# Kernel optimization log

Measured on AMD Instinct MI355X. Metric: run time of the kernel, lower is better.

Reference implementation:

```python
import jax, jax.numpy as jnp
import numpy as np

N = 50000          # nodes
E = 800000         # edges
D_IN, D_HID, D_OUT = 256, 128, 64
NUM_GRAPHS = 16
BN_EPS = 1e-5


def gcn_conv(x, src, dst, W, b, n_nodes):
    """PyG GCNConv: add self-loops, sym-normalized aggregation, then bias."""
    loop = jnp.arange(n_nodes, dtype=src.dtype)
    s = jnp.concatenate([src, loop])
    d = jnp.concatenate([dst, loop])
    deg = jax.ops.segment_sum(jnp.ones_like(s, dtype=x.dtype), d, num_segments=n_nodes)
    dinv = jax.lax.rsqrt(jnp.maximum(deg, 1.0))  # deg >= 1 due to self-loops
    norm = dinv[s] * dinv[d]                      # [E+N]
    h = x @ W                                     # [N, out]
    msg = h[s] * norm[:, None]                    # gather + scale
    out = jax.ops.segment_sum(msg, d, num_segments=n_nodes)
    return out + b


def batch_norm(x, gamma, beta):
    mu = jnp.mean(x, axis=0)
    var = jnp.mean(jnp.square(x - mu), axis=0)
    return (x - mu) * jax.lax.rsqrt(var + BN_EPS) * gamma + beta


def setup_inputs() -> dict:
    key = jax.random.key(0)
    ks = jax.random.split(key, 10)
    x = jax.random.normal(ks[0], (N, D_IN), dtype=jnp.float32)
    edge_index = jax.random.randint(ks[1], (2, E), 0, N, dtype=jnp.int64)
    batch = jnp.sort(jax.random.randint(ks[2], (N,), 0, NUM_GRAPHS, dtype=jnp.int64))
    def glorot(k, fan_in, fan_out):
        lim = np.sqrt(6.0 / (fan_in + fan_out))
        return jax.random.uniform(k, (fan_in, fan_out), jnp.float32, -lim, lim)
    return {
        "x": x, "edge_index": edge_index, "batch": batch,
        "W1": glorot(ks[3], D_IN, D_HID),  "b1": jnp.zeros((D_HID,), jnp.float32),
        "W2": glorot(ks[4], D_HID, D_HID), "b2": jnp.zeros((D_HID,), jnp.float32),
        "W3": glorot(ks[5], D_HID, D_OUT), "b3": jnp.zeros((D_OUT,), jnp.float32),
        "g1": jnp.ones((D_HID,), jnp.float32), "be1": jnp.zeros((D_HID,), jnp.float32),
        "g2": jnp.ones((D_HID,), jnp.float32), "be2": jnp.zeros((D_HID,), jnp.float32),
    }


def reference(x, edge_index, batch, W1, b1, W2, b2, W3, b3, g1, be1, g2, be2):
    src, dst = edge_index[0], edge_index[1]
    n = x.shape[0]
    h = gcn_conv(x, src, dst, W1, b1, n)
    h = jax.nn.relu(batch_norm(h, g1, be1))
    h = gcn_conv(h, src, dst, W2, b2, n)
    h = jax.nn.relu(batch_norm(h, g2, be2))
    h = gcn_conv(h, src, dst, W3, b3, n)          # [N, D_OUT]
    # global mean pool over graph ids
    sums = jax.ops.segment_sum(h, batch, num_segments=NUM_GRAPHS)
    cnts = jax.ops.segment_sum(jnp.ones((n,), h.dtype), batch, num_segments=NUM_GRAPHS)
    return sums / jnp.maximum(cnts, 1.0)[:, None]  # [NUM_GRAPHS, D_OUT]
```

## Files before the change

kernel.cpp:

```cpp
#include <hip/hip_runtime.h>
#include <hip/hip_bf16.h>

#define D_IN   256
#define D_HID  128
#define D_OUT_ 64
#define NGRAPH 16
#define BN_EPS 1e-5f

#define SCAN_TPB 256
#define SCAN_VPT 4

typedef __attribute__((ext_vector_type(8))) short short8;
typedef __attribute__((ext_vector_type(4))) float floatx4;

__device__ __forceinline__ unsigned short f2bf(float x) {
    unsigned u = __float_as_uint(x);
    return (unsigned short)((u + 0x7fffu + ((u >> 16) & 1u)) >> 16);
}
__device__ __forceinline__ unsigned pack2bf(float lo, float hi) {
    return (unsigned)f2bf(lo) | ((unsigned)f2bf(hi) << 16);
}
__device__ __forceinline__ void bf2_decode(unsigned u, float& lo, float& hi) {
    lo = __uint_as_float(u << 16);
    hi = __uint_as_float(u & 0xffff0000u);
}
__device__ __forceinline__ void accum8(float* acc, uint4 qv, float wt) {
    float f0,f1,f2,f3,f4,f5,f6,f7;
    bf2_decode(qv.x, f0, f1); bf2_decode(qv.y, f2, f3);
    bf2_decode(qv.z, f4, f5); bf2_decode(qv.w, f6, f7);
    acc[0]=fmaf(f0,wt,acc[0]); acc[1]=fmaf(f1,wt,acc[1]);
    acc[2]=fmaf(f2,wt,acc[2]); acc[3]=fmaf(f3,wt,acc[3]);
    acc[4]=fmaf(f4,wt,acc[4]); acc[5]=fmaf(f5,wt,acc[5]);
    acc[6]=fmaf(f6,wt,acc[6]); acc[7]=fmaf(f7,wt,acc[7]);
}

__global__ void count_deg_kernel(const int* __restrict__ dst, int E, int* __restrict__ deg) {
    int e = blockIdx.x * blockDim.x + threadIdx.x;
    if (e < E) atomicAdd(&deg[dst[e]], 1);
}

__global__ void dinv_kernel(const int* __restrict__ deg, int N, float* __restrict__ dinv) {
    int v = blockIdx.x * blockDim.x + threadIdx.x;
    if (v < N) dinv[v] = rsqrtf((float)(deg[v] + 1));
}

__global__ void block_sum_kernel(const int* __restrict__ deg, int N, int* __restrict__ bsum) {
    __shared__ int red[SCAN_TPB];
    int t = threadIdx.x;
    int base = blockIdx.x * (SCAN_TPB * SCAN_VPT) + t;
    int s = 0;
    #pragma unroll
    for (int i = 0; i < SCAN_VPT; ++i) {
        int idx = base + i * SCAN_TPB;
        if (idx < N) s += deg[idx];
    }
    red[t] = s;
    __syncthreads();
    for (int off = SCAN_TPB / 2; off > 0; off >>= 1) {
        if (t < off) red[t] += red[t + off];
        __syncthreads();
    }
    if (t == 0) bsum[blockIdx.x] = red[0];
}

__global__ void scan_bsum_kernel(const int* __restrict__ bsum, int NB,
                                 int* __restrict__ bprefix,
                                 int* __restrict__ rowstart, int N, int E) {
    __shared__ int part[SCAN_TPB];
    int t = threadIdx.x;
    int s = (t < NB) ? bsum[t] : 0;
    part[t] = s;
    __syncthreads();
    for (int off = 1; off < SCAN_TPB; off <<= 1) {
        int x = (t >= off) ? part[t - off] : 0;
        __syncthreads();
        part[t] += x;
        __syncthreads();
    }
    if (t < NB) bprefix[t] = part[t] - s;
    if (t == 0) rowstart[N] = E;
}

__global__ void local_scan_kernel(const int* __restrict__ deg, int N,
                                  const int* __restrict__ bprefix,
                                  int* __restrict__ rowstart) {
    __shared__ int part[SCAN_TPB];
    int t = threadIdx.x;
    int base = blockIdx.x * (SCAN_TPB * SCAN_VPT) + t * SCAN_VPT;
    int v[SCAN_VPT];
    int s = 0;
    #pragma unroll
    for (int i = 0; i < SCAN_VPT; ++i) {
        v[i] = (base + i < N) ? deg[base + i] : 0;
        s += v[i];
    }
    part[t] = s;
    __syncthreads();
    for (int off = 1; off < SCAN_TPB; off <<= 1) {
        int x = (t >= off) ? part[t - off] : 0;
        __syncthreads();
        part[t] += x;
        __syncthreads();
    }
    int excl = part[t] - s + bprefix[blockIdx.x];
    #pragma unroll
    for (int i = 0; i < SCAN_VPT; ++i) {
        if (base + i < N) rowstart[base + i] = excl;
        excl += v[i];
    }
}

__global__ void wprep_kernel(const float* __restrict__ W, int K, int NOUT,
                             unsigned short* __restrict__ Wt) {
    int idx = blockIdx.x * blockDim.x + threadIdx.x;
    if (idx >= K * NOUT) return;
    int k = idx / NOUT, n = idx - k * NOUT;
    Wt[(size_t)n * K + k] = f2bf(W[idx]);
}

template<int K, int NOUT, int FUSE, int ABF16>
__device__ __forceinline__ void gemm_body(
        int bid, const void* __restrict__ Aptr, const unsigned short* __restrict__ Wt,
        unsigned short* __restrict__ Cb, int M,
        const float* __restrict__ scale, const float* __restrict__ shift) {
    constexpr int NT = NOUT / 16;
    constexpr int KS = K / 32;
    int lane = threadIdx.x & 63;
    int wave = threadIdx.x >> 6;
    int col  = lane & 15;
    int quad = lane >> 4;
    int kq   = quad * 8;
    int row  = bid * 64 + wave * 16 + col;
    int rowc = min(row, M - 1);

    short8 afr[KS];
    if (ABF16) {
        const unsigned short* Ab = (const unsigned short*)Aptr;
        uint4 q[KS];
        #pragma unroll
        for (int i = 0; i < KS; ++i)
            q[i] = *(const uint4*)&Ab[(size_t)rowc * K + i * 32 + kq];
        #pragma unroll
        for (int i = 0; i < KS; ++i) {
            if (FUSE) {
                int kb = i * 32 + kq;
                float f0,f1,f2,f3,f4,f5,f6,f7;
                bf2_decode(q[i].x, f0, f1); bf2_decode(q[i].y, f2, f3);
                bf2_decode(q[i].z, f4, f5); bf2_decode(q[i].w, f6, f7);
                float4 sc0 = *(const float4*)&scale[kb];
                float4 sc1 = *(const float4*)&scale[kb + 4];
                float4 sh0 = *(const float4*)&shift[kb];
                float4 sh1 = *(const float4*)&shift[kb + 4];
                f0 = fmaxf(0.f, fmaf(f0, sc0.x, sh0.x));
                f1 = fmaxf(0.f, fmaf(f1, sc0.y, sh0.y));
                f2 = fmaxf(0.f, fmaf(f2, sc0.z, sh0.z));
                f3 = fmaxf(0.f, fmaf(f3, sc0.w, sh0.w));
                f4 = fmaxf(0.f, fmaf(f4, sc1.x, sh1.x));
                f5 = fmaxf(0.f, fmaf(f5, sc1.y, sh1.y));
                f6 = fmaxf(0.f, fmaf(f6, sc1.z, sh1.z));
                f7 = fmaxf(0.f, fmaf(f7, sc1.w, sh1.w));
                uint4 p;
                p.x = pack2bf(f0, f1); p.y = pack2bf(f2, f3);
                p.z = pack2bf(f4, f5); p.w = pack2bf(f6, f7);
                afr[i] = __builtin_bit_cast(short8, p);
            } else {
                afr[i] = __builtin_bit_cast(short8, q[i]);
            }
        }
    } else {
        const float* Af = (const float*)Aptr;
        float4 a0[KS], a1[KS];
        #pragma unroll
        for (int i = 0; i < KS; ++i) {
            a0[i] = *(const float4*)&Af[(size_t)rowc * K + i * 32 + kq];
            a1[i] = *(const float4*)&Af[(size_t)rowc * K + i * 32 + kq + 4];
        }
        #pragma unroll
        for (int i = 0; i < KS; ++i) {
            uint4 p;
            p.x = pack2bf(a0[i].x, a0[i].y); p.y = pack2bf(a0[i].z, a0[i].w);
            p.z = pack2bf(a1[i].x, a1[i].y); p.w = pack2bf(a1[i].z, a1[i].w);
            afr[i] = __builtin_bit_cast(short8, p);
        }
    }

    floatx4 acc[NT];
    #pragma unroll
    for (int nt = 0; nt < NT; ++nt) acc[nt] = (floatx4){0.f, 0.f, 0.f, 0.f};

    #pragma unroll
    for (int i = 0; i < KS; ++i) {
        #pragma unroll
        for (int nt = 0; nt < NT; ++nt) {
            short8 bfrag = *(const short8*)&Wt[(size_t)(nt * 16 + col) * K + i * 32 + kq];
            acc[nt] = __builtin_amdgcn_mfma_f32_16x16x32_bf16(afr[i], bfrag, acc[nt], 0, 0, 0);
        }
    }

    int obase = bid * 64 + wave * 16 + quad * 4;
    #pragma unroll
    for (int r = 0; r < 4; ++r) {
        int orow = obase + r;
        if (orow < M) {
            #pragma unroll
            for (int nt = 0; nt < NT; ++nt)
                Cb[(size_t)orow * NOUT + nt * 16 + col] = f2bf(acc[nt][r]);
        }
    }
}

template<int K, int NOUT, int FUSE, int ABF16>
__global__ __launch_bounds__(256) void gemm_mfma_kernel(
        const void* __restrict__ Aptr, const unsigned short* __restrict__ Wt,
        unsigned short* __restrict__ Cb, int M,
        const float* __restrict__ scale, const float* __restrict__ shift) {
    gemm_body<K, NOUT, FUSE, ABF16>(blockIdx.x, Aptr, Wt, Cb, M, scale, shift);
}

__global__ __launch_bounds__(256) void gemm1_scatter_kernel(
        const float* __restrict__ x, const unsigned short* __restrict__ Wt1,
        unsigned short* __restrict__ Cb, int M, int GB,
        const int* __restrict__ src, const int* __restrict__ dst, int E,
        const int* __restrict__ rowstart, int* __restrict__ cursor,
        const float* __restrict__ dinv, int2* __restrict__ csr) {
    if ((int)blockIdx.x < GB) {
        gemm_body<D_IN, D_HID, 0, 0>(blockIdx.x, x, Wt1, Cb, M, nullptr, nullptr);
    } else {
        int e = ((int)blockIdx.x - GB) * 256 + threadIdx.x;
        if (e < E) {
            int s = src[e], d = dst[e];
            int pos = rowstart[d] + atomicAdd(&cursor[d], 1);
            csr[pos] = make_int2(s, __float_as_int(dinv[s] * dinv[d]));
        }
    }
}

template<int D>
__global__ __launch_bounds__(256) void agg_bf16_kernel(
        const unsigned short* __restrict__ h, const float* __restrict__ dinv,
        const int* __restrict__ rowstart, const int2* __restrict__ csr,
        const float* __restrict__ bias,
        unsigned short* __restrict__ outb, int N) {
    constexpr int LPR = D / 8;
    constexpr int RPB = 256 / LPR;
    int lane = threadIdx.x & (LPR - 1);
    int r    = threadIdx.x / LPR;
    int v = blockIdx.x * RPB + r;
    if (v >= N) return;
    int c0 = lane * 8;
    const unsigned short* hc = h + c0;

    float acc[8];
    {
        float dv = dinv[v];
        float w = dv * dv;
        uint4 q = *(const uint4*)&hc[(size_t)v * D];
        float4 b0 = *(const float4*)&bias[c0];
        float4 b1 = *(const float4*)&bias[c0 + 4];
        acc[0]=b0.x; acc[1]=b0.y; acc[2]=b0.z; acc[3]=b0.w;
        acc[4]=b1.x; acc[5]=b1.y; acc[6]=b1.z; acc[7]=b1.w;
        accum8(acc, q, w);
    }

    int j  = rowstart[v];
    int j1 = rowstart[v + 1];
    for (; j + 4 <= j1; j += 4) {
        int2 r0 = csr[j],     r1 = csr[j + 1];
        int2 r2 = csr[j + 2], r3 = csr[j + 3];
        uint4 q0 = *(const uint4*)&hc[(size_t)r0.x * D];
        uint4 q1 = *(const uint4*)&hc[(size_t)r1.x * D];
        uint4 q2 = *(const uint4*)&hc[(size_t)r2.x * D];
        uint4 q3 = *(const uint4*)&hc[(size_t)r3.x * D];
        accum8(acc, q0, __int_as_float(r0.y)); accum8(acc, q1, __int_as_float(r1.y));
        accum8(acc, q2, __int_as_float(r2.y)); accum8(acc, q3, __int_as_float(r3.y));
    }
    for (; j < j1; ++j) {
        int2 rc = csr[j];
        uint4 q = *(const uint4*)&hc[(size_t)rc.x * D];
        accum8(acc, q, __int_as_float(rc.y));
    }

    uint4 o;
    o.x = pack2bf(acc[0], acc[1]); o.y = pack2bf(acc[2], acc[3]);
    o.z = pack2bf(acc[4], acc[5]); o.w = pack2bf(acc[6], acc[7]);
    *(uint4*)&outb[(size_t)v * D + c0] = o;
}

__global__ void bn_stats_bf16_kernel(const unsigned short* __restrict__ x, int N,
                                     float* __restrict__ sums, float* __restrict__ sumsq) {
    __shared__ float ls0[256], ls1[256], lq0[256], lq1[256];
    int pr = threadIdx.x & 63;
    int rg = threadIdx.x >> 6;
    float s0=0.f, s1=0.f, q0=0.f, q1=0.f;
    for (int v = blockIdx.x * 4 + rg; v < N; v += gridDim.x * 4) {
        unsigned u = *(const unsigned*)&x[(size_t)v * 128 + pr * 2];
        float lo, hi; bf2_decode(u, lo, hi);
        s0 += lo; s1 += hi;
        q0 = fmaf(lo, lo, q0); q1 = fmaf(hi, hi, q1);
    }
    ls0[threadIdx.x]=s0; ls1[threadIdx.x]=s1; lq0[threadIdx.x]=q0; lq1[threadIdx.x]=q1;
    __syncthreads();
    if (threadIdx.x < 64) {
        int pp = threadIdx.x;
        float a0=0,a1=0,b0=0,b1=0;
        #pragma unroll
        for (int g = 0; g < 4; ++g) {
            a0 += ls0[g*64+pp]; a1 += ls1[g*64+pp];
            b0 += lq0[g*64+pp]; b1 += lq1[g*64+pp];
        }
        atomicAdd(&sums[pp*2],  a0); atomicAdd(&sums[pp*2+1],  a1);
        atomicAdd(&sumsq[pp*2], b0); atomicAdd(&sumsq[pp*2+1], b1);
    }
}

__global__ void bn_final_kernel(const float* __restrict__ sums, const float* __restrict__ sumsq,
                                const float* __restrict__ g, const float* __restrict__ be,
                                int N, float* __restrict__ scale, float* __restrict__ shift) {
    int c = threadIdx.x;
    float inv_n = 1.0f / (float)N;
    float mu  = sums[c] * inv_n;
    float var = sumsq[c] * inv_n - mu * mu;
    float sc  = g[c] * rsqrtf(var + BN_EPS);
    scale[c] = sc;
    shift[c] = fmaf(-mu, sc, be[c]);
}

__global__ void pool_bf16_kernel(const unsigned short* __restrict__ x,
                                 const int* __restrict__ batch, int N,
                                 float* __restrict__ psum, int* __restrict__ pcnt) {
    __shared__ float ls[NGRAPH * 64];
    __shared__ int   lc[NGRAPH];
    for (int i = threadIdx.x; i < NGRAPH * 64; i += blockDim.x) ls[i] = 0.f;
    if (threadIdx.x < NGRAPH) lc[threadIdx.x] = 0;
    __syncthreads();
    int total = N * 32;
    for (int idx = blockIdx.x * blockDim.x + threadIdx.x; idx < total;
         idx += gridDim.x * blockDim.x) {
        int v = idx >> 5, cp = idx & 31;
        unsigned u = *(const unsigned*)&x[(size_t)v * 64 + cp * 2];
        float lo, hi; bf2_decode(u, lo, hi);
        int g = batch[v];
        atomicAdd(&ls[g * 64 + cp * 2],     lo);
        atomicAdd(&ls[g * 64 + cp * 2 + 1], hi);
        if (cp == 0) atomicAdd(&lc[g], 1);
    }
    __syncthreads();
    for (int i = threadIdx.x; i < NGRAPH * 64; i += blockDim.x) atomicAdd(&psum[i], ls[i]);
    if (threadIdx.x < NGRAPH) atomicAdd(&pcnt[threadIdx.x], lc[threadIdx.x]);
}

__global__ void pool_final_kernel(const float* __restrict__ psum, const int* __restrict__ pcnt,
                                  float* __restrict__ out) {
    int i = threadIdx.x;
    int g = i >> 6;
    float cnt = (float)max(pcnt[g], 1);
    out[i] = psum[i] / cnt;
}

extern "C" void kernel_launch(void* const* d_in, const int* in_sizes, int n_in,
                              void* d_out, int out_size, void* d_ws, size_t ws_size,
                              hipStream_t stream) {
    const float* x   = (const float*)d_in[0];
    const int*   ei  = (const int*)d_in[1];
    const int*   bat = (const int*)d_in[2];
    const float* W1  = (const float*)d_in[3];
    const float* b1  = (const float*)d_in[4];
    const float* W2  = (const float*)d_in[5];
    const float* b2  = (const float*)d_in[6];
    const float* W3  = (const float*)d_in[7];
    const float* b3  = (const float*)d_in[8];
    const float* g1  = (const float*)d_in[9];
    const float* be1 = (const float*)d_in[10];
    const float* g2  = (const float*)d_in[11];
    const float* be2 = (const float*)d_in[12];
    float* out = (float*)d_out;

    int N = in_sizes[0] / D_IN;
    int E = in_sizes[1] / 2;
    const int* src = ei;
    const int* dst = ei + E;

    char* p = (char*)d_ws;
    auto alloc = [&](size_t bytes) { char* r = p; p += (bytes + 255) & ~(size_t)255; return r; };
    int NB = (N + SCAN_TPB * SCAN_VPT - 1) / (SCAN_TPB * SCAN_VPT);
    int*   deg      = (int*)  alloc((size_t)N * 4);
    int*   rowstart = (int*)  alloc((size_t)(N + 1) * 4);
    int*   cursor   = (int*)  alloc((size_t)N * 4);
    float* dinv     = (float*)alloc((size_t)N * 4);
    int*   bsum     = (int*)  alloc((size_t)NB * 4);
    int*   bprefix  = (int*)  alloc((size_t)NB * 4);
    int2*  csr      = (int2*) alloc((size_t)E * 8);
    unsigned short* hb16   = (unsigned short*)alloc((size_t)N * 128 * 2);
    unsigned short* aggb16 = (unsigned short*)alloc((size_t)N * 128 * 2);
    unsigned short* Wt1 = (unsigned short*)alloc((size_t)D_HID * D_IN * 2);
    unsigned short* Wt2 = (unsigned short*)alloc((size_t)D_HID * D_HID * 2);
    unsigned short* Wt3 = (unsigned short*)alloc((size_t)D_OUT_ * D_HID * 2);
    float* sums     = (float*)alloc(128 * 4);
    float* sumsq    = (float*)alloc(128 * 4);
    float* scl      = (float*)alloc(128 * 4);
    float* shf      = (float*)alloc(128 * 4);
    float* psum     = (float*)alloc(NGRAPH * 64 * 4);
    int*   pcnt     = (int*)  alloc(NGRAPH * 4);

    int tpb = 256;
    int ebl = (E + tpb - 1) / tpb;
    int nbl = (N + tpb - 1) / tpb;
    int gblocks = (N + 63) / 64;

    wprep_kernel<<<(D_IN * D_HID + 255) / 256, 256, 0, stream>>>(W1, D_IN, D_HID, Wt1);
    wprep_kernel<<<(D_HID * D_HID + 255) / 256, 256, 0, stream>>>(W2, D_HID, D_HID, Wt2);
    wprep_kernel<<<(D_HID * D_OUT_ + 255) / 256, 256, 0, stream>>>(W3, D_HID, D_OUT_, Wt3);

    (void)hipMemsetAsync(deg, 0, (size_t)N * 4, stream);
    (void)hipMemsetAsync(cursor, 0, (size_t)N * 4, stream);
    count_deg_kernel<<<ebl, tpb, 0, stream>>>(dst, E, deg);
    dinv_kernel<<<nbl, tpb, 0, stream>>>(deg, N, dinv);
    block_sum_kernel<<<NB, SCAN_TPB, 0, stream>>>(deg, N, bsum);
    scan_bsum_kernel<<<1, SCAN_TPB, 0, stream>>>(bsum, NB, bprefix, rowstart, N, E);
    local_scan_kernel<<<NB, SCAN_TPB, 0, stream>>>(deg, N, bprefix, rowstart);

    gemm1_scatter_kernel<<<gblocks + ebl, 256, 0, stream>>>(
        x, Wt1, hb16, N, gblocks, src, dst, E, rowstart, cursor, dinv, csr);

    agg_bf16_kernel<D_HID><<<(N + 15) / 16, 256, 0, stream>>>(
        hb16, dinv, rowstart, csr, b1, aggb16, N);
    (void)hipMemsetAsync(sums, 0, 128 * 4, stream);
    (void)hipMemsetAsync(sumsq, 0, 128 * 4, stream);
    bn_stats_bf16_kernel<<<256, 256, 0, stream>>>(aggb16, N, sums, sumsq);
    bn_final_kernel<<<1, 128, 0, stream>>>(sums, sumsq, g1, be1, N, scl, shf);

    gemm_mfma_kernel<D_HID, D_HID, 1, 1><<<gblocks, 256, 0, stream>>>(
        aggb16, Wt2, hb16, N, scl, shf);
    agg_bf16_kernel<D_HID><<<(N + 15) / 16, 256, 0, stream>>>(
        hb16, dinv, rowstart, csr, b2, aggb16, N);
    (void)hipMemsetAsync(sums, 0, 128 * 4, stream);
    (void)hipMemsetAsync(sumsq, 0, 128 * 4, stream);
    bn_stats_bf16_kernel<<<256, 256, 0, stream>>>(aggb16, N, sums, sumsq);
    bn_final_kernel<<<1, 128, 0, stream>>>(sums, sumsq, g2, be2, N, scl, shf);

    gemm_mfma_kernel<D_HID, D_OUT_, 1, 1><<<gblocks, 256, 0, stream>>>(
        aggb16, Wt3, hb16, N, scl, shf);
    agg_bf16_kernel<D_OUT_><<<(N + 31) / 32, 256, 0, stream>>>(
        hb16, dinv, rowstart, csr, b3, aggb16, N);

    (void)hipMemsetAsync(psum, 0, NGRAPH * 64 * 4, stream);
    (void)hipMemsetAsync(pcnt, 0, NGRAPH * 4, stream);
    pool_bf16_kernel<<<256, 256, 0, stream>>>(aggb16, bat, N, psum, pcnt);
    pool_final_kernel<<<1, NGRAPH * 64, 0, stream>>>(psum, pcnt, out);
}
```

Measured before the change: 419.3 us.

## Shrink CSR to source ids, fold BN finalize into GEMM, batch scatter

The CSR entries drop the precomputed edge weight and store only the source index. The aggregation kernels now rebuild each weight from dinv[src]*dinv[dst], which halves CSR traffic and removes the dinv gathers from the scatter. The separate bn_final kernel launches are removed: each fused GEMM block computes scale and shift from the sums into shared memory. The edge scatter now handles four edges per thread, and its blocks are placed before the GEMM blocks. The cost is an extra random dinv gather per edge in every aggregation pass and a redundant per-block BN finalize.

```diff
diff --git a/kernel.cpp b/kernel.cpp
--- a/kernel.cpp
+++ b/kernel.cpp
@@ -122,9 +122,23 @@
 __device__ __forceinline__ void gemm_body(
         int bid, const void* __restrict__ Aptr, const unsigned short* __restrict__ Wt,
         unsigned short* __restrict__ Cb, int M,
-        const float* __restrict__ scale, const float* __restrict__ shift) {
+        const float* __restrict__ sums, const float* __restrict__ sumsq,
+        const float* __restrict__ gam, const float* __restrict__ bet, float invN) {
     constexpr int NT = NOUT / 16;
     constexpr int KS = K / 32;
+    __shared__ float s_sc[FUSE ? K : 1];
+    __shared__ float s_sh[FUSE ? K : 1];
+    if (FUSE) {
+        int t = threadIdx.x;
+        if (t < K) {
+            float mu  = sums[t] * invN;
+            float var = sumsq[t] * invN - mu * mu;
+            float sc  = gam[t] * rsqrtf(var + BN_EPS);
+            s_sc[t] = sc;
+            s_sh[t] = fmaf(-mu, sc, bet[t]);
+        }
+        __syncthreads();
+    }
     int lane = threadIdx.x & 63;
     int wave = threadIdx.x >> 6;
     int col  = lane & 15;
@@ -147,10 +161,10 @@
                 float f0,f1,f2,f3,f4,f5,f6,f7;
                 bf2_decode(q[i].x, f0, f1); bf2_decode(q[i].y, f2, f3);
                 bf2_decode(q[i].z, f4, f5); bf2_decode(q[i].w, f6, f7);
-                float4 sc0 = *(const float4*)&scale[kb];
-                float4 sc1 = *(const float4*)&scale[kb + 4];
-                float4 sh0 = *(const float4*)&shift[kb];
-                float4 sh1 = *(const float4*)&shift[kb + 4];
+                float4 sc0 = *(const float4*)&s_sc[kb];
+                float4 sc1 = *(const float4*)&s_sc[kb + 4];
+                float4 sh0 = *(const float4*)&s_sh[kb];
+                float4 sh1 = *(const float4*)&s_sh[kb + 4];
                 f0 = fmaxf(0.f, fmaf(f0, sc0.x, sh0.x));
                 f1 = fmaxf(0.f, fmaf(f1, sc0.y, sh0.y));
                 f2 = fmaxf(0.f, fmaf(f2, sc0.z, sh0.z));
@@ -213,32 +227,42 @@
 __global__ __launch_bounds__(256) void gemm_mfma_kernel(
         const void* __restrict__ Aptr, const unsigned short* __restrict__ Wt,
         unsigned short* __restrict__ Cb, int M,
-        const float* __restrict__ scale, const float* __restrict__ shift) {
-    gemm_body<K, NOUT, FUSE, ABF16>(blockIdx.x, Aptr, Wt, Cb, M, scale, shift);
+        const float* __restrict__ sums, const float* __restrict__ sumsq,
+        const float* __restrict__ gam, const float* __restrict__ bet, float invN) {
+    gemm_body<K, NOUT, FUSE, ABF16>(blockIdx.x, Aptr, Wt, Cb, M, sums, sumsq, gam, bet, invN);
 }
 
 __global__ __launch_bounds__(256) void gemm1_scatter_kernel(
         const float* __restrict__ x, const unsigned short* __restrict__ Wt1,
-        unsigned short* __restrict__ Cb, int M, int GB,
+        unsigned short* __restrict__ Cb, int M, int SB,
         const int* __restrict__ src, const int* __restrict__ dst, int E,
         const int* __restrict__ rowstart, int* __restrict__ cursor,
-        const float* __restrict__ dinv, int2* __restrict__ csr) {
-    if ((int)blockIdx.x < GB) {
-        gemm_body<D_IN, D_HID, 0, 0>(blockIdx.x, x, Wt1, Cb, M, nullptr, nullptr);
+        int* __restrict__ csr) {
+    if ((int)blockIdx.x < SB) {
+        int base = (int)blockIdx.x * 1024 + threadIdx.x;
+        int s[4], d[4];
+        #pragma unroll
+        for (int i = 0; i < 4; ++i) {
+            int e = base + i * 256;
+            if (e < E) { s[i] = src[e]; d[i] = dst[e]; } else { d[i] = -1; }
+        }
+        int pos[4];
+        #pragma unroll
+        for (int i = 0; i < 4; ++i)
+            if (d[i] >= 0) pos[i] = rowstart[d[i]] + atomicAdd(&cursor[d[i]], 1);
+        #pragma unroll
+        for (int i = 0; i < 4; ++i)
+            if (d[i] >= 0) csr[pos[i]] = s[i];
     } else {
-        int e = ((int)blockIdx.x - GB) * 256 + threadIdx.x;
-        if (e < E) {
-            int s = src[e], d = dst[e];
-            int pos = rowstart[d] + atomicAdd(&cursor[d], 1);
-            csr[pos] = make_int2(s, __float_as_int(dinv[s] * dinv[d]));
-        }
+        gemm_body<D_IN, D_HID, 0, 0>((int)blockIdx.x - SB, x, Wt1, Cb, M,
+                                     nullptr, nullptr, nullptr, nullptr, 0.f);
     }
 }
 
 template<int D>
 __global__ __launch_bounds__(256) void agg_bf16_kernel(
         const unsigned short* __restrict__ h, const float* __restrict__ dinv,
-        const int* __restrict__ rowstart, const int2* __restrict__ csr,
+        const int* __restrict__ rowstart, const int* __restrict__ csr,
         const float* __restrict__ bias,
         unsigned short* __restrict__ outb, int N) {
     constexpr int LPR = D / 8;
@@ -249,10 +273,10 @@
     if (v >= N) return;
     int c0 = lane * 8;
     const unsigned short* hc = h + c0;
+    float dv = dinv[v];
 
     float acc[8];
     {
-        float dv = dinv[v];
         float w = dv * dv;
         uint4 q = *(const uint4*)&hc[(size_t)v * D];
         float4 b0 = *(const float4*)&bias[c0];
@@ -265,19 +289,22 @@
     int j  = rowstart[v];
     int j1 = rowstart[v + 1];
     for (; j + 4 <= j1; j += 4) {
-        int2 r0 = csr[j],     r1 = csr[j + 1];
-        int2 r2 = csr[j + 2], r3 = csr[j + 3];
-        uint4 q0 = *(const uint4*)&hc[(size_t)r0.x * D];
-        uint4 q1 = *(const uint4*)&hc[(size_t)r1.x * D];
-        uint4 q2 = *(const uint4*)&hc[(size_t)r2.x * D];
-        uint4 q3 = *(const uint4*)&hc[(size_t)r3.x * D];
-        accum8(acc, q0, __int_as_float(r0.y)); accum8(acc, q1, __int_as_float(r1.y));
-        accum8(acc, q2, __int_as_float(r2.y)); accum8(acc, q3, __int_as_float(r3.y));
+        int s0 = csr[j],     s1 = csr[j + 1];
+        int s2 = csr[j + 2], s3 = csr[j + 3];
+        float w0 = dinv[s0] * dv, w1 = dinv[s1] * dv;
+        float w2 = dinv[s2] * dv, w3 = dinv[s3] * dv;
+        uint4 q0 = *(const uint4*)&hc[(size_t)s0 * D];
+        uint4 q1 = *(const uint4*)&hc[(size_t)s1 * D];
+        uint4 q2 = *(const uint4*)&hc[(size_t)s2 * D];
+        uint4 q3 = *(const uint4*)&hc[(size_t)s3 * D];
+        accum8(acc, q0, w0); accum8(acc, q1, w1);
+        accum8(acc, q2, w2); accum8(acc, q3, w3);
     }
     for (; j < j1; ++j) {
-        int2 rc = csr[j];
-        uint4 q = *(const uint4*)&hc[(size_t)rc.x * D];
-        accum8(acc, q, __int_as_float(rc.y));
+        int s = csr[j];
+        float w = dinv[s] * dv;
+        uint4 q = *(const uint4*)&hc[(size_t)s * D];
+        accum8(acc, q, w);
     }
 
     uint4 o;
@@ -311,18 +338,6 @@
         atomicAdd(&sums[pp*2],  a0); atomicAdd(&sums[pp*2+1],  a1);
         atomicAdd(&sumsq[pp*2], b0); atomicAdd(&sumsq[pp*2+1], b1);
     }
-}
-
-__global__ void bn_final_kernel(const float* __restrict__ sums, const float* __restrict__ sumsq,
-                                const float* __restrict__ g, const float* __restrict__ be,
-                                int N, float* __restrict__ scale, float* __restrict__ shift) {
-    int c = threadIdx.x;
-    float inv_n = 1.0f / (float)N;
-    float mu  = sums[c] * inv_n;
-    float var = sumsq[c] * inv_n - mu * mu;
-    float sc  = g[c] * rsqrtf(var + BN_EPS);
-    scale[c] = sc;
-    shift[c] = fmaf(-mu, sc, be[c]);
 }
 
 __global__ void pool_bf16_kernel(const unsigned short* __restrict__ x,
@@ -389,7 +404,7 @@
     float* dinv     = (float*)alloc((size_t)N * 4);
     int*   bsum     = (int*)  alloc((size_t)NB * 4);
     int*   bprefix  = (int*)  alloc((size_t)NB * 4);
-    int2*  csr      = (int2*) alloc((size_t)E * 8);
+    int*   csr      = (int*)  alloc((size_t)E * 4);
     unsigned short* hb16   = (unsigned short*)alloc((size_t)N * 128 * 2);
     unsigned short* aggb16 = (unsigned short*)alloc((size_t)N * 128 * 2);
     unsigned short* Wt1 = (unsigned short*)alloc((size_t)D_HID * D_IN * 2);
@@ -397,8 +412,6 @@
     unsigned short* Wt3 = (unsigned short*)alloc((size_t)D_OUT_ * D_HID * 2);
     float* sums     = (float*)alloc(128 * 4);
     float* sumsq    = (float*)alloc(128 * 4);
-    float* scl      = (float*)alloc(128 * 4);
-    float* shf      = (float*)alloc(128 * 4);
     float* psum     = (float*)alloc(NGRAPH * 64 * 4);
     int*   pcnt     = (int*)  alloc(NGRAPH * 4);
 
@@ -406,6 +419,8 @@
     int ebl = (E + tpb - 1) / tpb;
     int nbl = (N + tpb - 1) / tpb;
     int gblocks = (N + 63) / 64;
+    int sblocks = (E + 1023) / 1024;
+    float invN = 1.0f / (float)N;
 
     wprep_kernel<<<(D_IN * D_HID + 255) / 256, 256, 0, stream>>>(W1, D_IN, D_HID, Wt1);
     wprep_kernel<<<(D_HID * D_HID + 255) / 256, 256, 0, stream>>>(W2, D_HID, D_HID, Wt2);
@@ -419,27 +434,25 @@
     scan_bsum_kernel<<<1, SCAN_TPB, 0, stream>>>(bsum, NB, bprefix, rowstart, N, E);
     local_scan_kernel<<<NB, SCAN_TPB, 0, stream>>>(deg, N, bprefix, rowstart);
 
-    gemm1_scatter_kernel<<<gblocks + ebl, 256, 0, stream>>>(
-        x, Wt1, hb16, N, gblocks, src, dst, E, rowstart, cursor, dinv, csr);
+    gemm1_scatter_kernel<<<sblocks + gblocks, 256, 0, stream>>>(
+        x, Wt1, hb16, N, sblocks, src, dst, E, rowstart, cursor, csr);
 
     agg_bf16_kernel<D_HID><<<(N + 15) / 16, 256, 0, stream>>>(
         hb16, dinv, rowstart, csr, b1, aggb16, N);
     (void)hipMemsetAsync(sums, 0, 128 * 4, stream);
     (void)hipMemsetAsync(sumsq, 0, 128 * 4, stream);
     bn_stats_bf16_kernel<<<256, 256, 0, stream>>>(aggb16, N, sums, sumsq);
-    bn_final_kernel<<<1, 128, 0, stream>>>(sums, sumsq, g1, be1, N, scl, shf);
 
     gemm_mfma_kernel<D_HID, D_HID, 1, 1><<<gblocks, 256, 0, stream>>>(
-        aggb16, Wt2, hb16, N, scl, shf);
+        aggb16, Wt2, hb16, N, sums, sumsq, g1, be1, invN);
     agg_bf16_kernel<D_HID><<<(N + 15) / 16, 256, 0, stream>>>(
         hb16, dinv, rowstart, csr, b2, aggb16, N);
     (void)hipMemsetAsync(sums, 0, 128 * 4, stream);
     (void)hipMemsetAsync(sumsq, 0, 128 * 4, stream);
     bn_stats_bf16_kernel<<<256, 256, 0, stream>>>(aggb16, N, sums, sumsq);
-    bn_final_kernel<<<1, 128, 0, stream>>>(sums, sumsq, g2, be2, N, scl, shf);
 
     gemm_mfma_kernel<D_HID, D_OUT_, 1, 1><<<gblocks, 256, 0, stream>>>(
-        aggb16, Wt3, hb16, N, scl, shf);
+        aggb16, Wt3, hb16, N, sums, sumsq, g2, be2, invN);
     agg_bf16_kernel<D_OUT_><<<(N + 31) / 32, 256, 0, stream>>>(
         hb16, dinv, rowstart, csr, b3, aggb16, N);
 
```

New measurement: 431.5 us. 2.9% more time.
